# Optimization experiments

Measured on AMD Instinct MI355X. Metric: run time of the kernel, lower is better.

Reference implementation:

```python
import jax, jax.numpy as jnp
import numpy as np

IN_DIM = 1024
OUT_DIM = 2048
GRID = 5   # kan_config.grid_size
K = 3      # kan_config.spline_order


def b_splines(x, grid, k):
    """Cox-de Boor recursion.
    x: (N, D), grid: (D, G+2k+1) extended knots. Returns (N, D, G+k) basis values."""
    x = x[..., None]              # (N, D, 1)
    g = grid[None, :, :]          # (1, D, M)
    # degree-0 indicator bases
    B = ((x >= g[..., :-1]) & (x < g[..., 1:])).astype(x.dtype)  # (N, D, M-1)
    for p in range(1, k + 1):
        left = (x - g[..., : -(p + 1)]) / (g[..., p:-1] - g[..., : -(p + 1)])
        right = (g[..., p + 1:] - x) / (g[..., p + 1:] - g[..., 1:-p])
        B = left * B[..., :-1] + right * B[..., 1:]
    return B  # (N, D, G+k)


def setup_inputs() -> dict:
    key = jax.random.key(0)
    k1, k2, k3 = jax.random.split(key, 3)
    # inputs kept inside the spline grid range [-1, 1]
    x = jax.random.uniform(k1, (4, 2048, IN_DIM), jnp.float32, -1.0, 1.0)
    # uniform extended grid over [-1, 1] with k extra knots on each side
    h = 2.0 / GRID
    g = jnp.arange(-K, GRID + K + 1, dtype=jnp.float32) * h - 1.0  # (G+2K+1,)
    grid = jnp.broadcast_to(g, (IN_DIM, GRID + 2 * K + 1)).astype(jnp.float32)
    coef = (jax.random.normal(k2, (IN_DIM, OUT_DIM, GRID + K), jnp.float32) * 0.1)
    scale_base = jax.random.normal(k3, (IN_DIM, OUT_DIM), jnp.float32) * 0.1 + (1.0 / np.sqrt(IN_DIM)).astype(np.float32)
    scale_sp = jnp.ones((IN_DIM, OUT_DIM), jnp.float32)
    return {"x": x, "grid": grid, "coef": coef, "scale_base": scale_base, "scale_sp": scale_sp}


def reference(x, grid, coef, scale_base, scale_sp):
    shp = x.shape
    xf = x.reshape(-1, shp[-1])                 # (N, D)
    B = b_splines(xf, grid, K)                  # (N, D, G+K)
    coef_s = coef * scale_sp[:, :, None]        # fold per-edge spline scale into coefficients
    spline = jnp.einsum('ndg,dog->no', B, coef_s)          # (N, O)
    base = jnp.einsum('nd,do->no', jax.nn.silu(xf), scale_base)  # (N, O)
    out = base + spline
    return out.reshape(shp[:-1] + (OUT_DIM,))
```

## Files before the change

### kernel.cpp

```cpp
#include <hip/hip_runtime.h>
#include <hip/hip_bf16.h>
#include <cstdint>

typedef unsigned short u16;
typedef __bf16 bf16x8 __attribute__((ext_vector_type(8)));
typedef float  f32x4  __attribute__((ext_vector_type(4)));

typedef const __attribute__((address_space(1))) void* gptr_t;
typedef __attribute__((address_space(3))) void*       sptr_t;

#define IN_DIM  1024
#define OUT_DIM 2048
#define NROWS   8192
#define NB      8
#define KTOT    (IN_DIM * 9)
#define KSPL    (IN_DIM * 8)

#define WT_O 16
#define WT_D 64
#define TR_BLOCKS ((NROWS / 64) * (IN_DIM / 64))
#define WT_BLOCKS ((OUT_DIM / WT_O) * (IN_DIM / WT_D))

__device__ __forceinline__ float rcp_fast(float v) { return __builtin_amdgcn_rcpf(v); }

__device__ __forceinline__ u16 f2b(float v) {
  uint32_t u = __float_as_uint(v);
  uint32_t r = (u + 0x7FFFu + ((u >> 16) & 1u)) >> 16;
  return (u16)r;
}

__device__ __forceinline__ uint32_t pkbf(float a, float b) {
  return (uint32_t)f2b(a) | ((uint32_t)f2b(b) << 16);
}

__device__ __forceinline__ uint4 basis_pack(float xval) {
  float tt = (xval + 1.0f) * 2.5f;
  float jf = floorf(tt);
  jf = fminf(fmaxf(jf, 0.0f), 4.0f);
  const float u = tt - jf;
  const int j = (int)jf;
  const float um = 1.0f - u;
  const float u2 = u * u, u3 = u2 * u;
  const float b0 = um * um * um * (1.0f / 6.0f);
  const float b1 = (3.0f * u3 - 6.0f * u2 + 4.0f) * (1.0f / 6.0f);
  const float b2 = (-3.0f * u3 + 3.0f * u2 + 3.0f * u + 1.0f) * (1.0f / 6.0f);
  const float b3 = u3 * (1.0f / 6.0f);
  const uint32_t e01 = pkbf(b0, b1), e23 = pkbf(b2, b3);
  const uint32_t o0 = e01 << 16;
  const uint32_t o12 = (e01 >> 16) | (e23 << 16);
  const uint32_t o3 = e23 >> 16;
  const int odd = j & 1, m = j >> 1;
  const uint32_t a0 = odd ? o0 : e01;
  const uint32_t a1 = odd ? o12 : e23;
  const uint32_t a2 = odd ? o3 : 0u;
  uint4 wv;
  wv.x = (m == 0) ? a0 : 0u;
  wv.y = (m == 1) ? a0 : ((m == 0) ? a1 : 0u);
  wv.z = (m == 2) ? a0 : ((m == 1) ? a1 : ((m == 0) ? a2 : 0u));
  wv.w = (m == 2) ? a1 : ((m == 1) ? a2 : 0u);
  return wv;
}

__global__ __launch_bounds__(256) void kan_prep(const float* __restrict__ x,
                                                const float* __restrict__ coef,
                                                const float* __restrict__ scale_base,
                                                const float* __restrict__ scale_sp,
                                                float* __restrict__ xT,
                                                u16* __restrict__ sil,
                                                u16* __restrict__ wt) {
  const int t = threadIdx.x;

  if (blockIdx.x < TR_BLOCKS) {
    __shared__ float tile[64][65];
    const int bi = blockIdx.x;
    const int n0 = (bi & 127) * 64;
    const int d0 = (bi >> 7) * 64;
    const int col = t & 63, rbase = t >> 6;
#pragma unroll
    for (int i = 0; i < 16; ++i) {
      const int r = rbase + i * 4;
      const float v = x[(size_t)(n0 + r) * IN_DIM + d0 + col];
      tile[r][col] = v;
      sil[(size_t)(n0 + r) * IN_DIM + d0 + col] =
          f2b(v * rcp_fast(1.0f + __expf(-v)));
    }
    __syncthreads();
#pragma unroll
    for (int i = 0; i < 16; ++i) {
      const int dd = rbase + i * 4;
      xT[(size_t)(d0 + dd) * NROWS + n0 + col] = tile[col][dd];
    }
  } else {
    __shared__ __align__(16) u16 tsp[WT_O][WT_D * 8 + 8];
    __shared__ __align__(16) u16 tsi[WT_O][WT_D + 8];
    const int bi = blockIdx.x - TR_BLOCKS;
    const int o0 = (bi % (OUT_DIM / WT_O)) * WT_O;
    const int d0 = (bi / (OUT_DIM / WT_O)) * WT_D;
    const int ol = t & (WT_O - 1), dl0 = t >> 4;
#pragma unroll
    for (int rep = 0; rep < WT_D / 16; ++rep) {
      const int dl = rep * 16 + dl0;
      const int d = d0 + dl, o = o0 + ol;
      const size_t doff = (size_t)d * OUT_DIM + o;
      const float ssp = scale_sp[doff];
      const float sbv = scale_base[doff];
      const float4* cp = (const float4*)(coef + doff * 8);
      float4 c0 = cp[0], c1 = cp[1];
      uint4 val;
      val.x = pkbf(c0.x * ssp, c0.y * ssp);
      val.y = pkbf(c0.z * ssp, c0.w * ssp);
      val.z = pkbf(c1.x * ssp, c1.y * ssp);
      val.w = pkbf(c1.z * ssp, c1.w * ssp);
      *(uint4*)&tsp[ol][dl * 8] = val;
      tsi[ol][dl] = f2b(sbv);
    }
    __syncthreads();
    for (int i = t; i < WT_O * 64; i += 256) {
      const int row = i >> 6, col = i & 63;
      *(uint4*)(wt + (size_t)(o0 + row) * KTOT + (size_t)(d0 + col) * 8) =
          *(const uint4*)&tsp[row][col * 8];
    }
    if (t < WT_O * 8) {
      const int row = t >> 3, col = t & 7;
      *(uint4*)(wt + (size_t)(o0 + row) * KTOT + KSPL + d0 + col * 8) =
          *(const uint4*)&tsi[row][col * 8];
    }
  }
}

__global__ __launch_bounds__(256) void kan_gemm(const float* __restrict__ xT,
                                                const u16* __restrict__ sil,
                                                const u16* __restrict__ Bt,
                                                float* __restrict__ C) {
  __shared__ __align__(16) u16 As[128 * 64];
  __shared__ __align__(16) u16 Bs[128 * 64];
  const int tid  = threadIdx.x;
  const int lane = tid & 63;
  const int w    = tid >> 6;
  const int wm   = w >> 1, wn = w & 1;
  const int q    = lane >> 4, m16 = lane & 15;
  const int gx = blockIdx.x, gy = blockIdx.y;

  f32x4 acc[4][4];
#pragma unroll
  for (int i = 0; i < 4; ++i)
#pragma unroll
    for (int j = 0; j < 4; ++j) acc[i][j] = (f32x4){0.f, 0.f, 0.f, 0.f};

  const int srow = lane >> 3;
  const int swzc = (lane & 7) ^ srow;
  const u16* gb0 = Bt + (size_t)(gx * 128) * KTOT + swzc * 8;
  const int r7 = m16 & 15 & 7;
  const int dgrp = tid >> 5;
  const int nh   = tid & 31;

  for (int kk = 0; kk < KTOT; kk += 64) {
#pragma unroll
    for (int i = 0; i < 4; ++i) {
      const int rg = w * 32 + i * 8;
      __builtin_amdgcn_global_load_lds((gptr_t)(gb0 + (size_t)(rg + srow) * KTOT + kk),
                                       (sptr_t)&Bs[rg * 64], 16, 0, 0);
    }
    if (kk < KSPL) {
      const int d = (kk >> 3) + dgrp;
      const float4 xv = *(const float4*)(xT + (size_t)d * NROWS + gy * 128 + nh * 4);
      const float xa[4] = {xv.x, xv.y, xv.z, xv.w};
#pragma unroll
      for (int r = 0; r < 4; ++r) {
        const int row = nh * 4 + r;
        const uint4 wv = basis_pack(xa[r]);
        *(uint4*)&As[row * 64 + ((dgrp ^ (row & 7)) * 8)] = wv;
      }
    } else {
      const int kb = kk - KSPL;
#pragma unroll
      for (int i = 0; i < 4; ++i) {
        const int rg = w * 32 + i * 8;
        __builtin_amdgcn_global_load_lds(
            (gptr_t)(sil + (size_t)(gy * 128 + rg + srow) * IN_DIM + kb + swzc * 8),
            (sptr_t)&As[rg * 64], 16, 0, 0);
      }
    }
    __syncthreads();
#pragma unroll
    for (int ks = 0; ks < 64; ks += 32) {
      const int pc = ((ks >> 3) + q) ^ r7;
      bf16x8 af[4], bf[4];
#pragma unroll
      for (int mt = 0; mt < 4; ++mt)
        af[mt] = *(const bf16x8*)&As[(wm * 64 + mt * 16 + m16) * 64 + pc * 8];
#pragma unroll
      for (int nt = 0; nt < 4; ++nt)
        bf[nt] = *(const bf16x8*)&Bs[(wn * 64 + nt * 16 + m16) * 64 + pc * 8];
#pragma unroll
      for (int mt = 0; mt < 4; ++mt)
#pragma unroll
        for (int nt = 0; nt < 4; ++nt)
          acc[mt][nt] = __builtin_amdgcn_mfma_f32_16x16x32_bf16(af[mt], bf[nt],
                                                                acc[mt][nt], 0, 0, 0);
    }
    __syncthreads();
  }

#pragma unroll
  for (int mt = 0; mt < 4; ++mt) {
    const int row0 = gy * 128 + wm * 64 + mt * 16 + q * 4;
#pragma unroll
    for (int nt = 0; nt < 4; ++nt) {
      const int col = gx * 128 + wn * 64 + nt * 16 + m16;
#pragma unroll
      for (int r = 0; r < 4; ++r)
        C[(size_t)(row0 + r) * OUT_DIM + col] = acc[mt][nt][r];
    }
  }
}

__global__ __launch_bounds__(256) void kan_fallback(const float* __restrict__ x,
                                                    const float* __restrict__ grid,
                                                    const float* __restrict__ coef,
                                                    const float* __restrict__ scale_base,
                                                    const float* __restrict__ scale_sp,
                                                    float* __restrict__ out) {
  __shared__ float bs[IN_DIM * 9];
  const int n = blockIdx.x;
  const int t = threadIdx.x;
#pragma unroll
  for (int dd = 0; dd < IN_DIM / 256; ++dd) {
    const int d = t + dd * 256;
    const float xv = x[(size_t)n * IN_DIM + d];
    float tt = (xv + 1.0f) * 2.5f;
    float jf = floorf(tt);
    jf = fminf(fmaxf(jf, 0.0f), 4.0f);
    const float u = tt - jf;
    const int j = (int)jf;
    const float um = 1.0f - u;
    const float u2 = u * u, u3 = u2 * u;
    float* r = &bs[d * 9];
#pragma unroll
    for (int g = 0; g < NB; ++g) r[g] = 0.0f;
    r[j]     = um * um * um * (1.0f / 6.0f);
    r[j + 1] = (3.0f * u3 - 6.0f * u2 + 4.0f) * (1.0f / 6.0f);
    r[j + 2] = (-3.0f * u3 + 3.0f * u2 + 3.0f * u + 1.0f) * (1.0f / 6.0f);
    r[j + 3] = u3 * (1.0f / 6.0f);
    r[8]     = xv * rcp_fast(1.0f + __expf(-xv));
  }
  __syncthreads();
  const int o = blockIdx.y * 256 + t;
  float acc = 0.0f;
  for (int d = 0; d < IN_DIM; ++d) {
    const size_t doff = (size_t)d * OUT_DIM + o;
    const float4* cp = (const float4*)(coef + doff * 8);
    float4 c0 = cp[0], c1 = cp[1];
    const float* b = &bs[d * 9];
    float s = b[0] * c0.x + b[1] * c0.y + b[2] * c0.z + b[3] * c0.w +
              b[4] * c1.x + b[5] * c1.y + b[6] * c1.z + b[7] * c1.w;
    acc += s * scale_sp[doff] + b[8] * scale_base[doff];
  }
  out[(size_t)n * OUT_DIM + o] = acc;
}

extern "C" void kernel_launch(void* const* d_in, const int* in_sizes, int n_in,
                              void* d_out, int out_size, void* d_ws, size_t ws_size,
                              hipStream_t stream) {
  const float* x  = (const float*)d_in[0];
  const float* gr = (const float*)d_in[1];
  const float* cf = (const float*)d_in[2];
  const float* sb = (const float*)d_in[3];
  const float* sp = (const float*)d_in[4];
  float* out = (float*)d_out;

  const size_t xT_bytes  = (size_t)IN_DIM * NROWS * sizeof(float);
  const size_t sil_bytes = (size_t)NROWS * IN_DIM * sizeof(u16);
  const size_t wt_bytes  = (size_t)OUT_DIM * KTOT * sizeof(u16);
  const size_t need = xT_bytes + sil_bytes + wt_bytes;

  if (ws_size >= need) {
    float* xT = (float*)d_ws;
    u16* sil  = (u16*)((char*)d_ws + xT_bytes);
    u16* wt   = (u16*)((char*)d_ws + xT_bytes + sil_bytes);
    kan_prep<<<dim3(TR_BLOCKS + WT_BLOCKS), dim3(256), 0, stream>>>(
        x, cf, sb, sp, xT, sil, wt);
    kan_gemm<<<dim3(OUT_DIM / 128, NROWS / 128), dim3(256), 0, stream>>>(
        xT, sil, wt, out);
  } else {
    kan_fallback<<<dim3(NROWS, OUT_DIM / 256), dim3(256), 0, stream>>>(x, gr, cf, sb, sp, out);
  }
}
```

Baseline: 524.2 us.

## Materialize bf16 basis activations and use a 256x256 four-stage LDS-pipelined MFMA GEMM

The prep kernel now writes the full bf16 activation matrix (8 packed B-spline basis values per input plus the SiLU term) directly, replacing the transposed fp32 x and separate SiLU buffer. A new GEMM kernel with 512 threads computes 256x256 output tiles using direct global-to-LDS loads, a 4-deep buffer ring with swizzled layout, and a remapped block order. This removes on-the-fly basis construction inside the GEMM. In exchange it writes and reads a larger activation buffer (about 150MB) and needs more workspace, and the old path remains as a fallback when workspace is too small.

```diff
diff --git a/kernel.cpp b/kernel.cpp
--- a/kernel.cpp
+++ b/kernel.cpp
@@ -20,6 +20,11 @@
 #define WT_D 64
 #define TR_BLOCKS ((NROWS / 64) * (IN_DIM / 64))
 #define WT_BLOCKS ((OUT_DIM / WT_O) * (IN_DIM / WT_D))
+#define ACT_BLOCKS ((NROWS / 64) * (IN_DIM / 64))
+
+#define BK 32
+#define TILE_U16 (256 * BK)
+#define NKT (KTOT / BK)
 
 __device__ __forceinline__ float rcp_fast(float v) { return __builtin_amdgcn_rcpf(v); }
 
@@ -61,39 +66,39 @@
   return wv;
 }
 
-__global__ __launch_bounds__(256) void kan_prep(const float* __restrict__ x,
-                                                const float* __restrict__ coef,
-                                                const float* __restrict__ scale_base,
-                                                const float* __restrict__ scale_sp,
-                                                float* __restrict__ xT,
-                                                u16* __restrict__ sil,
-                                                u16* __restrict__ wt) {
+__global__ __launch_bounds__(256) void kan_prep2(const float* __restrict__ x,
+                                                 const float* __restrict__ coef,
+                                                 const float* __restrict__ scale_base,
+                                                 const float* __restrict__ scale_sp,
+                                                 u16* __restrict__ act,
+                                                 u16* __restrict__ wt) {
   const int t = threadIdx.x;
 
-  if (blockIdx.x < TR_BLOCKS) {
-    __shared__ float tile[64][65];
+  if (blockIdx.x < ACT_BLOCKS) {
+    __shared__ __align__(16) u16 st[64][72];
     const int bi = blockIdx.x;
     const int n0 = (bi & 127) * 64;
     const int d0 = (bi >> 7) * 64;
-    const int col = t & 63, rbase = t >> 6;
+    const int dl = t & 63, r0 = t >> 6;
 #pragma unroll
     for (int i = 0; i < 16; ++i) {
-      const int r = rbase + i * 4;
-      const float v = x[(size_t)(n0 + r) * IN_DIM + d0 + col];
-      tile[r][col] = v;
-      sil[(size_t)(n0 + r) * IN_DIM + d0 + col] =
-          f2b(v * rcp_fast(1.0f + __expf(-v)));
-    }
-    __syncthreads();
-#pragma unroll
-    for (int i = 0; i < 16; ++i) {
-      const int dd = rbase + i * 4;
-      xT[(size_t)(d0 + dd) * NROWS + n0 + col] = tile[col][dd];
+      const int r = r0 + i * 4;
+      const float v = x[(size_t)(n0 + r) * IN_DIM + d0 + dl];
+      *(uint4*)&act[(size_t)(n0 + r) * KTOT + (size_t)(d0 + dl) * 8] = basis_pack(v);
+      st[r][dl] = f2b(v * rcp_fast(1.0f + __expf(-v)));
+    }
+    __syncthreads();
+#pragma unroll
+    for (int j = 0; j < 2; ++j) {
+      const int idx = t + j * 256;
+      const int r = idx >> 3, c8 = idx & 7;
+      *(uint4*)&act[(size_t)(n0 + r) * KTOT + KSPL + d0 + c8 * 8] =
+          *(const uint4*)&st[r][c8 * 8];
     }
   } else {
     __shared__ __align__(16) u16 tsp[WT_O][WT_D * 8 + 8];
     __shared__ __align__(16) u16 tsi[WT_O][WT_D + 8];
-    const int bi = blockIdx.x - TR_BLOCKS;
+    const int bi = blockIdx.x - ACT_BLOCKS;
     const int o0 = (bi % (OUT_DIM / WT_O)) * WT_O;
     const int d0 = (bi / (OUT_DIM / WT_O)) * WT_D;
     const int ol = t & (WT_O - 1), dl0 = t >> 4;
@@ -128,6 +133,184 @@
   }
 }
 
+__global__ __launch_bounds__(512, 2) void kan_gemm2(const u16* __restrict__ act,
+                                                    const u16* __restrict__ Bt,
+                                                    float* __restrict__ C) {
+  __shared__ __align__(16) u16 As[4 * TILE_U16];
+  __shared__ __align__(16) u16 Bs[4 * TILE_U16];
+  const int tid  = threadIdx.x;
+  const int lane = tid & 63;
+  const int w    = tid >> 6;
+  const int wm   = w >> 2, wn = w & 3;
+  const int q    = lane >> 4, m16 = lane & 15;
+
+  const int bid = (blockIdx.x & 7) * 32 + (blockIdx.x >> 3);
+  const int gx = bid & 7;
+  const int gy = bid >> 3;
+
+  f32x4 acc[8][4];
+#pragma unroll
+  for (int i = 0; i < 8; ++i)
+#pragma unroll
+    for (int j = 0; j < 4; ++j) acc[i][j] = (f32x4){0.f, 0.f, 0.f, 0.f};
+
+  const int rA  = lane >> 2;
+  const int csw = ((lane & 3) ^ ((lane >> 3) & 3)) * 8;
+  const u16* gA = act + (size_t)(gy * 256 + w * 32 + rA) * KTOT + csw;
+  const u16* gB = Bt  + (size_t)(gx * 256 + w * 32 + rA) * KTOT + csw;
+  const int ldsw = w * 1024;
+
+#define STAGE(T)                                                               \
+  do {                                                                         \
+    const int _buf = (T) & 3;                                                  \
+    const size_t _k0 = (size_t)(T) * BK;                                       \
+    const u16* _ga = gA + _k0;                                                 \
+    const u16* _gb = gB + _k0;                                                 \
+    u16* _la = &As[_buf * TILE_U16 + ldsw];                                    \
+    u16* _lb = &Bs[_buf * TILE_U16 + ldsw];                                    \
+    __builtin_amdgcn_global_load_lds((gptr_t)_ga, (sptr_t)_la, 16, 0, 0);      \
+    __builtin_amdgcn_global_load_lds((gptr_t)(_ga + (size_t)16 * KTOT),        \
+                                     (sptr_t)(_la + 512), 16, 0, 0);           \
+    __builtin_amdgcn_global_load_lds((gptr_t)_gb, (sptr_t)_lb, 16, 0, 0);      \
+    __builtin_amdgcn_global_load_lds((gptr_t)(_gb + (size_t)16 * KTOT),        \
+                                     (sptr_t)(_lb + 512), 16, 0, 0);           \
+  } while (0)
+
+  const int px8 = (q ^ ((m16 >> 1) & 3)) * 8;
+  const int aoff = (wm * 128 + m16) * 32 + px8;
+  const int boff = (wn * 64 + m16) * 32 + px8;
+
+#define COMPUTE(T)                                                             \
+  do {                                                                         \
+    const int _buf = (T) & 3;                                                  \
+    const u16* _A = &As[_buf * TILE_U16 + aoff];                               \
+    const u16* _B = &Bs[_buf * TILE_U16 + boff];                               \
+    bf16x8 _bf[4];                                                             \
+    _Pragma("unroll") for (int nt = 0; nt < 4; ++nt)                           \
+        _bf[nt] = *(const bf16x8*)&_B[nt * 512];                               \
+    bf16x8 _af[8];                                                             \
+    _Pragma("unroll") for (int mt = 0; mt < 8; ++mt)                           \
+        _af[mt] = *(const bf16x8*)&_A[mt * 512];                               \
+    __builtin_amdgcn_s_setprio(1);                                             \
+    _Pragma("unroll") for (int mt = 0; mt < 8; ++mt)                           \
+      _Pragma("unroll") for (int nt = 0; nt < 4; ++nt)                         \
+          acc[mt][nt] = __builtin_amdgcn_mfma_f32_16x16x32_bf16(               \
+              _af[mt], _bf[nt], acc[mt][nt], 0, 0, 0);                         \
+    __builtin_amdgcn_s_setprio(0);                                             \
+  } while (0)
+
+#define KSTEP(T, VM, DOSTAGE)                                                  \
+  do {                                                                         \
+    if (DOSTAGE) STAGE((T) + 3);                                               \
+    asm volatile("s_waitcnt vmcnt(" #VM ")" ::: "memory");                     \
+    __builtin_amdgcn_s_barrier();                                              \
+    COMPUTE(T);                                                                \
+    asm volatile("" ::: "memory");                                             \
+    __builtin_amdgcn_s_barrier();                                              \
+  } while (0)
+
+  STAGE(0);
+  STAGE(1);
+  STAGE(2);
+
+  for (int tb = 0; tb < 71; ++tb) {
+#pragma unroll
+    for (int j = 0; j < 4; ++j) {
+      const int t = tb * 4 + j;
+      KSTEP(t, 12, true);
+    }
+  }
+  KSTEP(284, 12, true);
+  KSTEP(285, 8, false);
+  KSTEP(286, 4, false);
+  KSTEP(287, 0, false);
+
+#undef KSTEP
+#undef COMPUTE
+#undef STAGE
+
+  const int row_base = gy * 256 + wm * 128 + q * 4;
+  const int col_base = gx * 256 + wn * 64 + m16;
+#pragma unroll
+  for (int mt = 0; mt < 8; ++mt) {
+#pragma unroll
+    for (int nt = 0; nt < 4; ++nt) {
+      const int r0 = row_base + mt * 16;
+      const int c  = col_base + nt * 16;
+#pragma unroll
+      for (int r = 0; r < 4; ++r)
+        C[(size_t)(r0 + r) * OUT_DIM + c] = acc[mt][nt][r];
+    }
+  }
+}
+
+__global__ __launch_bounds__(256) void kan_prep(const float* __restrict__ x,
+                                                const float* __restrict__ coef,
+                                                const float* __restrict__ scale_base,
+                                                const float* __restrict__ scale_sp,
+                                                float* __restrict__ xT,
+                                                u16* __restrict__ sil,
+                                                u16* __restrict__ wt) {
+  const int t = threadIdx.x;
+
+  if (blockIdx.x < TR_BLOCKS) {
+    __shared__ float tile[64][65];
+    const int bi = blockIdx.x;
+    const int n0 = (bi & 127) * 64;
+    const int d0 = (bi >> 7) * 64;
+    const int col = t & 63, rbase = t >> 6;
+#pragma unroll
+    for (int i = 0; i < 16; ++i) {
+      const int r = rbase + i * 4;
+      const float v = x[(size_t)(n0 + r) * IN_DIM + d0 + col];
+      tile[r][col] = v;
+      sil[(size_t)(n0 + r) * IN_DIM + d0 + col] =
+          f2b(v * rcp_fast(1.0f + __expf(-v)));
+    }
+    __syncthreads();
+#pragma unroll
+    for (int i = 0; i < 16; ++i) {
+      const int dd = rbase + i * 4;
+      xT[(size_t)(d0 + dd) * NROWS + n0 + col] = tile[col][dd];
+    }
+  } else {
+    __shared__ __align__(16) u16 tsp[WT_O][WT_D * 8 + 8];
+    __shared__ __align__(16) u16 tsi[WT_O][WT_D + 8];
+    const int bi = blockIdx.x - TR_BLOCKS;
+    const int o0 = (bi % (OUT_DIM / WT_O)) * WT_O;
+    const int d0 = (bi / (OUT_DIM / WT_O)) * WT_D;
+    const int ol = t & (WT_O - 1), dl0 = t >> 4;
+#pragma unroll
+    for (int rep = 0; rep < WT_D / 16; ++rep) {
+      const int dl = rep * 16 + dl0;
+      const int d = d0 + dl, o = o0 + ol;
+      const size_t doff = (size_t)d * OUT_DIM + o;
+      const float ssp = scale_sp[doff];
+      const float sbv = scale_base[doff];
+      const float4* cp = (const float4*)(coef + doff * 8);
+      float4 c0 = cp[0], c1 = cp[1];
+      uint4 val;
+      val.x = pkbf(c0.x * ssp, c0.y * ssp);
+      val.y = pkbf(c0.z * ssp, c0.w * ssp);
+      val.z = pkbf(c1.x * ssp, c1.y * ssp);
+      val.w = pkbf(c1.z * ssp, c1.w * ssp);
+      *(uint4*)&tsp[ol][dl * 8] = val;
+      tsi[ol][dl] = f2b(sbv);
+    }
+    __syncthreads();
+    for (int i = t; i < WT_O * 64; i += 256) {
+      const int row = i >> 6, col = i & 63;
+      *(uint4*)(wt + (size_t)(o0 + row) * KTOT + (size_t)(d0 + col) * 8) =
+          *(const uint4*)&tsp[row][col * 8];
+    }
+    if (t < WT_O * 8) {
+      const int row = t >> 3, col = t & 7;
+      *(uint4*)(wt + (size_t)(o0 + row) * KTOT + KSPL + d0 + col * 8) =
+          *(const uint4*)&tsi[row][col * 8];
+    }
+  }
+}
+
 __global__ __launch_bounds__(256) void kan_gemm(const float* __restrict__ xT,
                                                 const u16* __restrict__ sil,
                                                 const u16* __restrict__ Bt,
@@ -269,12 +452,21 @@
   const float* sp = (const float*)d_in[4];
   float* out = (float*)d_out;
 
+  const size_t act_bytes = (size_t)NROWS * KTOT * sizeof(u16);
+  const size_t wt_bytes  = (size_t)OUT_DIM * KTOT * sizeof(u16);
+  const size_t need1 = act_bytes + wt_bytes;
+
   const size_t xT_bytes  = (size_t)IN_DIM * NROWS * sizeof(float);
   const size_t sil_bytes = (size_t)NROWS * IN_DIM * sizeof(u16);
-  const size_t wt_bytes  = (size_t)OUT_DIM * KTOT * sizeof(u16);
-  const size_t need = xT_bytes + sil_bytes + wt_bytes;
-
-  if (ws_size >= need) {
+  const size_t need2 = xT_bytes + sil_bytes + wt_bytes;
+
+  if (ws_size >= need1) {
+    u16* act = (u16*)d_ws;
+    u16* wt  = (u16*)((char*)d_ws + act_bytes);
+    kan_prep2<<<dim3(ACT_BLOCKS + WT_BLOCKS), dim3(256), 0, stream>>>(
+        x, cf, sb, sp, act, wt);
+    kan_gemm2<<<dim3(256), dim3(512), 0, stream>>>(act, wt, out);
+  } else if (ws_size >= need2) {
     float* xT = (float*)d_ws;
     u16* sil  = (u16*)((char*)d_ws + xT_bytes);
     u16* wt   = (u16*)((char*)d_ws + xT_bytes + sil_bytes);
```

Measured after the change: 474.8 us. 1.1x faster.

## Rewrite GEMM with 256x256 tiles, 4-stage LDS pipeline and register prefetch

Applied to the files above, without the earlier changes.

Replaces the 128x128 single-buffered GEMM with a 512-thread, 256x256-tile kernel that uses a 4-deep LDS ring buffer with BK=32. Global-to-LDS loads for B run three tiles ahead, and the spline basis for A is computed two tiles ahead. MFMA fragments are prefetched from LDS while the current tile's MFMAs issue under raised wave priority. A block-index swizzle is added for L2 locality. The aim is to hide memory latency behind compute and to reduce global traffic per FLOP. In exchange, the larger tiles raise register pressure and leave only 256 blocks, so occupancy and CU balance become a risk.

```diff
diff --git a/kernel.cpp b/kernel.cpp
--- a/kernel.cpp
+++ b/kernel.cpp
@@ -20,6 +20,10 @@
 #define WT_D 64
 #define TR_BLOCKS ((NROWS / 64) * (IN_DIM / 64))
 #define WT_BLOCKS ((OUT_DIM / WT_O) * (IN_DIM / WT_D))
+
+#define BK 32
+#define TILE_U16 (256 * BK)
+#define NKT (KTOT / BK)
 
 __device__ __forceinline__ float rcp_fast(float v) { return __builtin_amdgcn_rcpf(v); }
 
@@ -128,89 +132,189 @@
   }
 }
 
-__global__ __launch_bounds__(256) void kan_gemm(const float* __restrict__ xT,
-                                                const u16* __restrict__ sil,
-                                                const u16* __restrict__ Bt,
-                                                float* __restrict__ C) {
-  __shared__ __align__(16) u16 As[128 * 64];
-  __shared__ __align__(16) u16 Bs[128 * 64];
+__global__ __launch_bounds__(512, 2) void kan_gemm3(const float* __restrict__ xT,
+                                                    const u16* __restrict__ sil,
+                                                    const u16* __restrict__ Bt,
+                                                    float* __restrict__ C) {
+  __shared__ __align__(16) u16 As[4 * TILE_U16];
+  __shared__ __align__(16) u16 Bs[4 * TILE_U16];
   const int tid  = threadIdx.x;
   const int lane = tid & 63;
   const int w    = tid >> 6;
-  const int wm   = w >> 1, wn = w & 1;
+  const int wm   = w >> 2, wn = w & 3;
   const int q    = lane >> 4, m16 = lane & 15;
-  const int gx = blockIdx.x, gy = blockIdx.y;
-
-  f32x4 acc[4][4];
-#pragma unroll
-  for (int i = 0; i < 4; ++i)
+
+  const int bid = (blockIdx.x & 7) * 32 + (blockIdx.x >> 3);
+  const int gx = bid & 7;
+  const int gy = bid >> 3;
+
+  f32x4 acc[8][4];
+#pragma unroll
+  for (int i = 0; i < 8; ++i)
 #pragma unroll
     for (int j = 0; j < 4; ++j) acc[i][j] = (f32x4){0.f, 0.f, 0.f, 0.f};
 
-  const int srow = lane >> 3;
-  const int swzc = (lane & 7) ^ srow;
-  const u16* gb0 = Bt + (size_t)(gx * 128) * KTOT + swzc * 8;
-  const int r7 = m16 & 15 & 7;
-  const int dgrp = tid >> 5;
-  const int nh   = tid & 31;
-
-  for (int kk = 0; kk < KTOT; kk += 64) {
-#pragma unroll
-    for (int i = 0; i < 4; ++i) {
-      const int rg = w * 32 + i * 8;
-      __builtin_amdgcn_global_load_lds((gptr_t)(gb0 + (size_t)(rg + srow) * KTOT + kk),
-                                       (sptr_t)&Bs[rg * 64], 16, 0, 0);
-    }
-    if (kk < KSPL) {
-      const int d = (kk >> 3) + dgrp;
-      const float4 xv = *(const float4*)(xT + (size_t)d * NROWS + gy * 128 + nh * 4);
-      const float xa[4] = {xv.x, xv.y, xv.z, xv.w};
-#pragma unroll
-      for (int r = 0; r < 4; ++r) {
-        const int row = nh * 4 + r;
-        const uint4 wv = basis_pack(xa[r]);
-        *(uint4*)&As[row * 64 + ((dgrp ^ (row & 7)) * 8)] = wv;
-      }
-    } else {
-      const int kb = kk - KSPL;
-#pragma unroll
-      for (int i = 0; i < 4; ++i) {
-        const int rg = w * 32 + i * 8;
-        __builtin_amdgcn_global_load_lds(
-            (gptr_t)(sil + (size_t)(gy * 128 + rg + srow) * IN_DIM + kb + swzc * 8),
-            (sptr_t)&As[rg * 64], 16, 0, 0);
-      }
-    }
-    __syncthreads();
-#pragma unroll
-    for (int ks = 0; ks < 64; ks += 32) {
-      const int pc = ((ks >> 3) + q) ^ r7;
-      bf16x8 af[4], bf[4];
-#pragma unroll
-      for (int mt = 0; mt < 4; ++mt)
-        af[mt] = *(const bf16x8*)&As[(wm * 64 + mt * 16 + m16) * 64 + pc * 8];
-#pragma unroll
-      for (int nt = 0; nt < 4; ++nt)
-        bf[nt] = *(const bf16x8*)&Bs[(wn * 64 + nt * 16 + m16) * 64 + pc * 8];
-#pragma unroll
-      for (int mt = 0; mt < 4; ++mt)
-#pragma unroll
-        for (int nt = 0; nt < 4; ++nt)
-          acc[mt][nt] = __builtin_amdgcn_mfma_f32_16x16x32_bf16(af[mt], bf[nt],
-                                                                acc[mt][nt], 0, 0, 0);
-    }
-    __syncthreads();
-  }
-
-#pragma unroll
-  for (int mt = 0; mt < 4; ++mt) {
-    const int row0 = gy * 128 + wm * 64 + mt * 16 + q * 4;
+  const int rA  = lane >> 2;
+  const int csw = ((lane & 3) ^ ((lane >> 3) & 3)) * 8;
+  const u16* gB = Bt  + (size_t)(gx * 256 + w * 32 + rA) * KTOT + csw;
+  const u16* sA = sil + (size_t)(gy * 256 + w * 32 + rA) * IN_DIM + csw;
+  const int ldsw = w * 1024;
+
+  const int arow = tid & 255;
+  const int cd0  = tid >> 8;
+  const int asw  = (arow >> 1) & 3;
+  const int aw0  = arow * 32 + (cd0 ^ asw) * 8;
+  const int aw1  = arow * 32 + ((cd0 + 2) ^ asw) * 8;
+  const float* xp = xT + (size_t)cd0 * NROWS + gy * 256 + arow;
+
+#define STAGE_B(T)                                                             \
+  do {                                                                         \
+    const int _bb = (T) & 3;                                                   \
+    const size_t _k0 = (size_t)(T) * BK;                                       \
+    __builtin_amdgcn_global_load_lds((gptr_t)(gB + _k0),                       \
+        (sptr_t)&Bs[_bb * TILE_U16 + ldsw], 16, 0, 0);                         \
+    __builtin_amdgcn_global_load_lds((gptr_t)(gB + (size_t)16 * KTOT + _k0),   \
+        (sptr_t)&Bs[_bb * TILE_U16 + ldsw + 512], 16, 0, 0);                   \
+  } while (0)
+
+#define STAGE_A_SIL(T)                                                         \
+  do {                                                                         \
+    const int _ab = (T) & 3;                                                   \
+    const size_t _db = (size_t)(T) * BK - KSPL;                                \
+    __builtin_amdgcn_global_load_lds((gptr_t)(sA + _db),                       \
+        (sptr_t)&As[_ab * TILE_U16 + ldsw], 16, 0, 0);                         \
+    __builtin_amdgcn_global_load_lds((gptr_t)(sA + (size_t)16 * IN_DIM + _db), \
+        (sptr_t)&As[_ab * TILE_U16 + ldsw + 512], 16, 0, 0);                   \
+  } while (0)
+
+#define WRITE_A_SPL(T, X0, X1)                                                 \
+  do {                                                                         \
+    const int _ab = (T) & 3;                                                   \
+    *(uint4*)&As[_ab * TILE_U16 + aw0] = basis_pack(X0);                       \
+    *(uint4*)&As[_ab * TILE_U16 + aw1] = basis_pack(X1);                       \
+  } while (0)
+
+  const int px8 = (q ^ ((m16 >> 1) & 3)) * 8;
+  const int aoff = (wm * 128 + m16) * 32 + px8;
+  const int boff = (wn * 64 + m16) * 32 + px8;
+
+  bf16x8 fa[8], fb[4];
+
+#define CORE(T)                                                                \
+  do {                                                                         \
+    const u16* _An = &As[(((T) + 1) & 3) * TILE_U16 + aoff];                   \
+    const u16* _Bn = &Bs[(((T) + 1) & 3) * TILE_U16 + boff];                   \
+    __builtin_amdgcn_s_setprio(1);                                             \
+    _Pragma("unroll") for (int mt = 0; mt < 8; ++mt) {                         \
+      _Pragma("unroll") for (int nt = 0; nt < 4; ++nt)                         \
+        acc[mt][nt] = __builtin_amdgcn_mfma_f32_16x16x32_bf16(                 \
+            fa[mt], fb[nt], acc[mt][nt], 0, 0, 0);                             \
+      fa[mt] = *(const bf16x8*)&_An[mt * 512];                                 \
+    }                                                                          \
+    __builtin_amdgcn_s_setprio(0);                                             \
+    _Pragma("unroll") for (int nt = 0; nt < 4; ++nt)                           \
+      fb[nt] = *(const bf16x8*)&_Bn[nt * 512];                                 \
+  } while (0)
+
+#define ENDSYNC(VM)                                                            \
+  do {                                                                         \
+    asm volatile("s_waitcnt vmcnt(" #VM ")" ::: "memory");                     \
+    asm volatile("s_waitcnt lgkmcnt(0)" ::: "memory");                         \
+    __builtin_amdgcn_s_barrier();                                              \
+  } while (0)
+
+#define SP_REGION(T)                                                           \
+  do {                                                                         \
+    const float _x0 = xp[(size_t)(((T) + 2) * 4) * NROWS];                     \
+    const float _x1 = xp[(size_t)(((T) + 2) * 4 + 2) * NROWS];                 \
+    STAGE_B((T) + 3);                                                          \
+    CORE(T);                                                                   \
+    WRITE_A_SPL((T) + 2, _x0, _x1);                                            \
+    ENDSYNC(2);                                                                \
+  } while (0)
+
+#define SI_REGION(T)                                                           \
+  do {                                                                         \
+    STAGE_A_SIL((T) + 2);                                                      \
+    STAGE_B((T) + 3);                                                          \
+    CORE(T);                                                                   \
+    ENDSYNC(2);                                                                \
+  } while (0)
+
+  STAGE_B(0);
+  STAGE_B(1);
+  STAGE_B(2);
+  {
+    const float x00 = xp[0];
+    const float x01 = xp[(size_t)2 * NROWS];
+    const float x10 = xp[(size_t)4 * NROWS];
+    const float x11 = xp[(size_t)6 * NROWS];
+    WRITE_A_SPL(0, x00, x01);
+    WRITE_A_SPL(1, x10, x11);
+  }
+  ENDSYNC(2);
+  {
+    const u16* _A0 = &As[aoff];
+    const u16* _B0 = &Bs[boff];
+#pragma unroll
+    for (int nt = 0; nt < 4; ++nt) fb[nt] = *(const bf16x8*)&_B0[nt * 512];
+#pragma unroll
+    for (int mt = 0; mt < 8; ++mt) fa[mt] = *(const bf16x8*)&_A0[mt * 512];
+  }
+
+  for (int tb = 0; tb < 63; ++tb) {
+#pragma unroll
+    for (int j = 0; j < 4; ++j) {
+      SP_REGION(tb * 4 + j);
+    }
+  }
+  SP_REGION(252);
+  SP_REGION(253);
+
+  SI_REGION(254);
+  SI_REGION(255);
+  for (int tb = 0; tb < 7; ++tb) {
+#pragma unroll
+    for (int j = 0; j < 4; ++j) {
+      SI_REGION(256 + tb * 4 + j);
+    }
+  }
+  SI_REGION(284);
+
+  STAGE_A_SIL(287);
+  CORE(285);
+  ENDSYNC(0);
+  CORE(286);
+  asm volatile("s_waitcnt lgkmcnt(0)" ::: "memory");
+  __builtin_amdgcn_s_barrier();
+  __builtin_amdgcn_s_setprio(1);
+#pragma unroll
+  for (int mt = 0; mt < 8; ++mt)
+#pragma unroll
+    for (int nt = 0; nt < 4; ++nt)
+      acc[mt][nt] = __builtin_amdgcn_mfma_f32_16x16x32_bf16(fa[mt], fb[nt],
+                                                            acc[mt][nt], 0, 0, 0);
+  __builtin_amdgcn_s_setprio(0);
+
+#undef SP_REGION
+#undef SI_REGION
+#undef ENDSYNC
+#undef CORE
+#undef WRITE_A_SPL
+#undef STAGE_A_SIL
+#undef STAGE_B
+
+  const int row_base = gy * 256 + wm * 128 + q * 4;
+  const int col_base = gx * 256 + wn * 64 + m16;
+#pragma unroll
+  for (int mt = 0; mt < 8; ++mt) {
 #pragma unroll
     for (int nt = 0; nt < 4; ++nt) {
-      const int col = gx * 128 + wn * 64 + nt * 16 + m16;
+      const int r0 = row_base + mt * 16;
+      const int c  = col_base + nt * 16;
 #pragma unroll
       for (int r = 0; r < 4; ++r)
-        C[(size_t)(row0 + r) * OUT_DIM + col] = acc[mt][nt][r];
+        C[(size_t)(r0 + r) * OUT_DIM + c] = acc[mt][nt][r];
     }
   }
 }
@@ -280,8 +384,7 @@
     u16* wt   = (u16*)((char*)d_ws + xT_bytes + sil_bytes);
     kan_prep<<<dim3(TR_BLOCKS + WT_BLOCKS), dim3(256), 0, stream>>>(
         x, cf, sb, sp, xT, sil, wt);
-    kan_gemm<<<dim3(OUT_DIM / 128, NROWS / 128), dim3(256), 0, stream>>>(
-        xT, sil, wt, out);
+    kan_gemm3<<<dim3(256), dim3(512), 0, stream>>>(xT, sil, wt, out);
   } else {
     kan_fallback<<<dim3(NROWS, OUT_DIM / 256), dim3(256), 0, stream>>>(x, gr, cf, sb, sp, out);
   }
```

Measured after the change: 431.0 us. 1.22x faster.
